# Kernel tuning notes

Hardware: AMD Instinct MI355X
Metric: run time of the kernel (lower is better)

Reference implementation:

```python
import jax, jax.numpy as jnp
import numpy as np

B, T, D, H = 2, 2048, 1024, 16
HD = D // H  # 64
SCALE = 1.0 / np.sqrt(D).astype(np.float32)  # module uses 1/sqrt(mod_dim), not head_dim


def setup_inputs() -> dict:
    key = jax.random.key(0)
    k1, k2, k3 = jax.random.split(key, 3)
    x = jax.random.normal(k1, (B, T, D), dtype=jnp.float32)
    W_attn = jax.random.normal(k2, (3 * D, D), dtype=jnp.float32) * 0.02
    W_out = jax.random.normal(k3, (D, D), dtype=jnp.float32) * 0.02
    return {"x": x, "W_attn": W_attn, "W_out": W_out}


def reference(x, W_attn, W_out):
    b, t, d = x.shape
    # qkv projection (Linear, no bias): x @ W^T
    qkv = jnp.einsum('btd,ed->bte', x, W_attn)  # [b, t, 3d]
    q, k, v = jnp.split(qkv, 3, axis=-1)
    # [b, h, t, hd]
    q = q.reshape(b, t, H, HD).transpose(0, 2, 1, 3)
    k = k.reshape(b, t, H, HD).transpose(0, 2, 1, 3)
    v = v.reshape(b, t, H, HD).transpose(0, 2, 1, 3)
    # raw scores, causal mask applied before scaling (scale*-inf == -inf, so
    # equivalent to the original mask-then-scale order)
    att = jnp.einsum('bhqd,bhkd->bhqk', q, k)
    causal = jnp.tril(jnp.ones((t, t), dtype=bool))
    att = jnp.where(causal[None, None], att * SCALE, -jnp.inf)
    att = jax.nn.softmax(att, axis=-1)
    z = jnp.einsum('bhqk,bhkd->bhqd', att, v)
    z = z.transpose(0, 2, 1, 3).reshape(b, t, d)
    return jnp.einsum('btd,od->bto', z, W_out)
```

## Files before the change

### kernel.cpp

```cpp
#include <hip/hip_runtime.h>
#include <cstddef>

typedef unsigned short u16;
typedef __attribute__((ext_vector_type(4))) float floatx4;
typedef __attribute__((ext_vector_type(8))) short short8;

#define TT 2048
#define DD 1024
#define NH 16
#define ATT_SCALE (1.0f / 32.0f)
#define PSTR 72

__device__ __forceinline__ u16 f2bf(float f) {
  unsigned u = __builtin_bit_cast(unsigned, f);
  u += 0x7fffu + ((u >> 16) & 1u);
  return (u16)(u >> 16);
}

__device__ __forceinline__ unsigned pack2(float a, float b) {
#if __has_builtin(__builtin_amdgcn_cvt_pk_bf16_f32)
  auto t = __builtin_amdgcn_cvt_pk_bf16_f32(a, b);
  return __builtin_bit_cast(unsigned, t);
#else
  unsigned ua = __builtin_bit_cast(unsigned, a);
  ua += 0x7fffu + ((ua >> 16) & 1u);
  unsigned ub = __builtin_bit_cast(unsigned, b);
  ub += 0x7fffu + ((ub >> 16) & 1u);
  return (ua >> 16) | (ub & 0xffff0000u);
#endif
}

__device__ __forceinline__ void g2l16(const u16* g, u16* l) {
#if __has_builtin(__builtin_amdgcn_global_load_lds)
  __builtin_amdgcn_global_load_lds(
      (const __attribute__((address_space(1))) unsigned int*)g,
      (__attribute__((address_space(3))) unsigned int*)l, 16, 0, 0);
#else
  *(int4*)l = *(const int4*)g;
#endif
}

__device__ __forceinline__ short8 scale_q(short8 q) {
  short8 r;
#pragma unroll
  for (int i = 0; i < 8; ++i) {
    float f = __builtin_bit_cast(float, ((unsigned)(u16)q[i]) << 16) * ATT_SCALE;
    r[i] = (short)f2bf(f);
  }
  return r;
}

__global__ __launch_bounds__(256) void cvt3_kernel(const float* __restrict__ a,
                                                   const float* __restrict__ b,
                                                   const float* __restrict__ c,
                                                   u16* __restrict__ out,
                                                   int na, int nb, int nc) {
  int i = blockIdx.x * 256 + threadIdx.x;
  const float* src;
  int j;
  if (i < na) { src = a; j = i; }
  else if (i < na + nb) { src = b; j = i - na; }
  else if (i < na + nb + nc) { src = c; j = i - na - nb; }
  else return;
  float4 v = ((const float4*)src)[j];
  ((ushort4*)out)[i] = make_ushort4(f2bf(v.x), f2bf(v.y), f2bf(v.z), f2bf(v.w));
}

template <int MODE, int BN>
__global__ __launch_bounds__(256) void gemm_bt(const u16* __restrict__ A,
                                               const u16* __restrict__ Bm,
                                               void* __restrict__ C,
                                               u16* __restrict__ vt,
                                               int M, int N, int K) {
  constexpr int NT = BN / 32;
  __shared__ u16 As[128 * 32];
  __shared__ u16 Bs[BN * 32];
  const int tid = threadIdx.x;
  const int lane = tid & 63;
  const int wave = tid >> 6;
  const int quad = lane >> 4;
  const int l16 = lane & 15;
  const int wm = (wave >> 1) * 64;
  const int wn = (wave & 1) * (BN / 2);
  const int m0 = blockIdx.x * 128;
  const int n0 = blockIdx.y * BN;

  const int srow = wave * 16 + (lane >> 2);
  const int scol = (lane & 3) * 8;
  const int sl = wave * 512 + lane * 8;

  floatx4 acc[4][NT] = {};

  for (int k0 = 0; k0 < K; k0 += 32) {
    __syncthreads();
    g2l16(&A[(size_t)(m0 + srow) * K + k0 + scol], &As[sl]);
    g2l16(&A[(size_t)(m0 + 64 + srow) * K + k0 + scol], &As[2048 + sl]);
    g2l16(&Bm[(size_t)(n0 + srow) * K + k0 + scol], &Bs[sl]);
    if (BN == 128)
      g2l16(&Bm[(size_t)(n0 + 64 + srow) * K + k0 + scol], &Bs[2048 + sl]);
    __syncthreads();

    short8 af[4];
#pragma unroll
    for (int mt = 0; mt < 4; ++mt)
      af[mt] = *(const short8*)&As[(wm + mt * 16 + l16) * 32 + quad * 8];
#pragma unroll
    for (int nt = 0; nt < NT; ++nt) {
      short8 bf = *(const short8*)&Bs[(wn + nt * 16 + l16) * 32 + quad * 8];
#pragma unroll
      for (int mt = 0; mt < 4; ++mt)
        acc[mt][nt] = __builtin_amdgcn_mfma_f32_16x16x32_bf16(af[mt], bf, acc[mt][nt], 0, 0, 0);
    }
  }

  if (MODE == 2 && n0 >= 2048) {
    const int bidx = m0 >> 11;
    const int tbase = (m0 & 2047) + wm;
#pragma unroll
    for (int mt = 0; mt < 4; ++mt)
#pragma unroll
      for (int nt = 0; nt < NT; ++nt) {
        int gn = n0 + wn + nt * 16 + l16;
        size_t vrow = (size_t)(bidx * 1024 + gn - 2048);
        int t = tbase + mt * 16 + quad * 4;
        uint2 val;
        val.x = pack2(acc[mt][nt][0], acc[mt][nt][1]);
        val.y = pack2(acc[mt][nt][2], acc[mt][nt][3]);
        *(uint2*)&vt[vrow * TT + t] = val;
      }
  } else {
    const int cw = (MODE == 2) ? 2048 : N;
#pragma unroll
    for (int mt = 0; mt < 4; ++mt)
#pragma unroll
      for (int nt = 0; nt < NT; ++nt)
#pragma unroll
        for (int r = 0; r < 4; ++r) {
          int gm = m0 + wm + mt * 16 + quad * 4 + r;
          int gn = n0 + wn + nt * 16 + l16;
          float v = acc[mt][nt][r];
          if (MODE >= 1)
            ((u16*)C)[(size_t)gm * cw + gn] = f2bf(v);
          else
            ((float*)C)[(size_t)gm * cw + gn] = v;
        }
  }
}

__global__ __launch_bounds__(512) void attn_flash5(const u16* __restrict__ qk,
                                                   const u16* __restrict__ vt,
                                                   u16* __restrict__ z) {
  __shared__ u16 Ks[2][64 * PSTR];
  __shared__ u16 Vs[2][64 * PSTR];
  __shared__ u16 Ps[8][16 * PSTR];

  const int tid = threadIdx.x;
  const int lane = tid & 63;
  const int wave = tid >> 6;
  const int qs = wave & 3;
  const int par = wave >> 2;
  const int quad = lane >> 4;
  const int l16 = lane & 15;

  const int p = blockIdx.x;
  const int qtA = p, qtB = 31 - p;
  const int bh = blockIdx.y;
  const int b = bh >> 4, h = bh & 15;

  const size_t bbase = (size_t)b * TT * 2048;
  const u16* qg = qk + bbase + h * 64;
  const u16* kg = qk + bbase + 1024 + h * 64;
  const u16* vtg = vt + (size_t)bh * 64 * TT;

  short8 qfA[2], qfB[2];
  {
    const size_t ra = (size_t)(qtA * 64 + qs * 16 + l16) * 2048;
    const size_t rb = (size_t)(qtB * 64 + qs * 16 + l16) * 2048;
    qfA[0] = scale_q(*(const short8*)&qg[ra + quad * 8]);
    qfA[1] = scale_q(*(const short8*)&qg[ra + 32 + quad * 8]);
    qfB[0] = scale_q(*(const short8*)&qg[rb + quad * 8]);
    qfB[1] = scale_q(*(const short8*)&qg[rb + 32 + quad * 8]);
  }

  floatx4 OA[4] = {}, OB[4] = {};
  float psA[4] = {}, psB[4] = {};

  const int tsel = tid >> 8;
  const int t8 = tid & 255;
  const int str = t8 >> 2, sc = (t8 & 3) * 16;

  const int nktB = qtB + 1;
  const int M = (nktB + 1) >> 1;
  const int qrbA = qtA * 64 + qs * 16 + quad * 4;
  const int qrbB = qtB * 64 + qs * 16 + quad * 4;

  for (int m = 0; m < M; ++m) {
    const int kt = 2 * m + par;
    const int kt0 = kt * 64;
    __syncthreads();
    {
      const int kst = 2 * m + tsel;
      if (kst < nktB) {
        *(int4*)&Ks[tsel][str * PSTR + sc] =
            *(const int4*)&kg[(size_t)(kst * 64 + str) * 2048 + sc];
        *(int4*)&Ks[tsel][str * PSTR + sc + 8] =
            *(const int4*)&kg[(size_t)(kst * 64 + str) * 2048 + sc + 8];
        *(int4*)&Vs[tsel][str * PSTR + sc] =
            *(const int4*)&vtg[(size_t)str * TT + kst * 64 + sc];
        *(int4*)&Vs[tsel][str * PSTR + sc + 8] =
            *(const int4*)&vtg[(size_t)str * TT + kst * 64 + sc + 8];
      }
    }
    __syncthreads();

    if (kt < nktB) {
      floatx4 s[4];
#pragma unroll
      for (int nt = 0; nt < 4; ++nt) {
        short8 k0 = *(const short8*)&Ks[par][(nt * 16 + l16) * PSTR + quad * 8];
        short8 k1 = *(const short8*)&Ks[par][(nt * 16 + l16) * PSTR + 32 + quad * 8];
        floatx4 zz = {0.f, 0.f, 0.f, 0.f};
        s[nt] = __builtin_amdgcn_mfma_f32_16x16x32_bf16(qfB[0], k0, zz, 0, 0, 0);
        s[nt] = __builtin_amdgcn_mfma_f32_16x16x32_bf16(qfB[1], k1, s[nt], 0, 0, 0);
      }
      if (kt == qtB) {
#pragma unroll
        for (int nt = 0; nt < 4; ++nt)
#pragma unroll
          for (int r = 0; r < 4; ++r) {
            int kk = kt0 + nt * 16 + l16;
            float pv = (kk <= qrbB + r) ? __expf(s[nt][r]) : 0.f;
            psB[r] += pv;
            Ps[wave][(quad * 4 + r) * PSTR + nt * 16 + l16] = f2bf(pv);
          }
      } else {
#pragma unroll
        for (int nt = 0; nt < 4; ++nt)
#pragma unroll
          for (int r = 0; r < 4; ++r) {
            float pv = __expf(s[nt][r]);
            psB[r] += pv;
            Ps[wave][(quad * 4 + r) * PSTR + nt * 16 + l16] = f2bf(pv);
          }
      }
      {
        short8 p0 = *(const short8*)&Ps[wave][l16 * PSTR + quad * 8];
        short8 p1 = *(const short8*)&Ps[wave][l16 * PSTR + 32 + quad * 8];
#pragma unroll
        for (int nt = 0; nt < 4; ++nt) {
          short8 v0 = *(const short8*)&Vs[par][(nt * 16 + l16) * PSTR + quad * 8];
          short8 v1 = *(const short8*)&Vs[par][(nt * 16 + l16) * PSTR + 32 + quad * 8];
          OB[nt] = __builtin_amdgcn_mfma_f32_16x16x32_bf16(p0, v0, OB[nt], 0, 0, 0);
          OB[nt] = __builtin_amdgcn_mfma_f32_16x16x32_bf16(p1, v1, OB[nt], 0, 0, 0);
        }
      }

      if (kt <= qtA) {
#pragma unroll
        for (int nt = 0; nt < 4; ++nt) {
          short8 k0 = *(const short8*)&Ks[par][(nt * 16 + l16) * PSTR + quad * 8];
          short8 k1 = *(const short8*)&Ks[par][(nt * 16 + l16) * PSTR + 32 + quad * 8];
          floatx4 zz = {0.f, 0.f, 0.f, 0.f};
          s[nt] = __builtin_amdgcn_mfma_f32_16x16x32_bf16(qfA[0], k0, zz, 0, 0, 0);
          s[nt] = __builtin_amdgcn_mfma_f32_16x16x32_bf16(qfA[1], k1, s[nt], 0, 0, 0);
        }
        if (kt == qtA) {
#pragma unroll
          for (int nt = 0; nt < 4; ++nt)
#pragma unroll
            for (int r = 0; r < 4; ++r) {
              int kk = kt0 + nt * 16 + l16;
              float pv = (kk <= qrbA + r) ? __expf(s[nt][r]) : 0.f;
              psA[r] += pv;
              Ps[wave][(quad * 4 + r) * PSTR + nt * 16 + l16] = f2bf(pv);
            }
        } else {
#pragma unroll
          for (int nt = 0; nt < 4; ++nt)
#pragma unroll
            for (int r = 0; r < 4; ++r) {
              float pv = __expf(s[nt][r]);
              psA[r] += pv;
              Ps[wave][(quad * 4 + r) * PSTR + nt * 16 + l16] = f2bf(pv);
            }
        }
        short8 p0 = *(const short8*)&Ps[wave][l16 * PSTR + quad * 8];
        short8 p1 = *(const short8*)&Ps[wave][l16 * PSTR + 32 + quad * 8];
#pragma unroll
        for (int nt = 0; nt < 4; ++nt) {
          short8 v0 = *(const short8*)&Vs[par][(nt * 16 + l16) * PSTR + quad * 8];
          short8 v1 = *(const short8*)&Vs[par][(nt * 16 + l16) * PSTR + 32 + quad * 8];
          OA[nt] = __builtin_amdgcn_mfma_f32_16x16x32_bf16(p0, v0, OA[nt], 0, 0, 0);
          OA[nt] = __builtin_amdgcn_mfma_f32_16x16x32_bf16(p1, v1, OA[nt], 0, 0, 0);
        }
      }
    }
  }

#pragma unroll
  for (int off = 1; off < 16; off <<= 1)
#pragma unroll
    for (int r = 0; r < 4; ++r) {
      psA[r] += __shfl_xor(psA[r], off, 64);
      psB[r] += __shfl_xor(psB[r], off, 64);
    }

  float* red = (float*)Ps;
  float* lred = red + 4096;
  __syncthreads();
  if (par == 1) {
#pragma unroll
    for (int nt = 0; nt < 4; ++nt)
#pragma unroll
      for (int r = 0; r < 4; ++r)
        red[(qs * 16 + quad * 4 + r) * 64 + nt * 16 + l16] = OA[nt][r];
    if (l16 == 0)
#pragma unroll
      for (int r = 0; r < 4; ++r) lred[qs * 16 + quad * 4 + r] = psA[r];
  }
  __syncthreads();
  if (par == 0) {
#pragma unroll
    for (int r = 0; r < 4; ++r) {
      int row = qs * 16 + quad * 4 + r;
      float rl = 1.0f / (psA[r] + lred[row]);
      int qa = qtA * 64 + row;
#pragma unroll
      for (int nt = 0; nt < 4; ++nt) {
        float o = OA[nt][r] + red[row * 64 + nt * 16 + l16];
        z[(size_t)(b * TT + qa) * DD + h * 64 + nt * 16 + l16] = f2bf(o * rl);
      }
    }
  }
  __syncthreads();
  if (par == 1) {
#pragma unroll
    for (int nt = 0; nt < 4; ++nt)
#pragma unroll
      for (int r = 0; r < 4; ++r)
        red[(qs * 16 + quad * 4 + r) * 64 + nt * 16 + l16] = OB[nt][r];
    if (l16 == 0)
#pragma unroll
      for (int r = 0; r < 4; ++r) lred[qs * 16 + quad * 4 + r] = psB[r];
  }
  __syncthreads();
  if (par == 0) {
#pragma unroll
    for (int r = 0; r < 4; ++r) {
      int row = qs * 16 + quad * 4 + r;
      float rl = 1.0f / (psB[r] + lred[row]);
      int qb = qtB * 64 + row;
#pragma unroll
      for (int nt = 0; nt < 4; ++nt) {
        float o = OB[nt][r] + red[row * 64 + nt * 16 + l16];
        z[(size_t)(b * TT + qb) * DD + h * 64 + nt * 16 + l16] = f2bf(o * rl);
      }
    }
  }
}

extern "C" void kernel_launch(void* const* d_in, const int* in_sizes, int n_in,
                              void* d_out, int out_size, void* d_ws, size_t ws_size,
                              hipStream_t stream) {
  const float* x  = (const float*)d_in[0];
  const float* Wa = (const float*)d_in[1];
  const float* Wo = (const float*)d_in[2];
  float* out = (float*)d_out;

  u16* xb  = (u16*)d_ws;
  u16* Wab = xb  + (size_t)4096 * 1024;
  u16* Wob = Wab + (size_t)3072 * 1024;
  u16* qk  = Wob + (size_t)1024 * 1024;
  u16* z   = qk  + (size_t)4096 * 2048;
  u16* vt  = z   + (size_t)4096 * 1024;

  cvt3_kernel<<<8192, 256, 0, stream>>>(x, Wa, Wo, xb, 1048576, 786432, 262144);

  gemm_bt<2, 128><<<dim3(32, 24), 256, 0, stream>>>(xb, Wab, qk, vt, 4096, 3072, 1024);

  attn_flash5<<<dim3(16, 2 * NH), 512, 0, stream>>>(qk, vt, z);

  gemm_bt<0, 64><<<dim3(32, 16), 256, 0, stream>>>(z, Wob, out, nullptr, 4096, 1024, 1024);
}
```

Measured before the change: 179.3 us.

## Keep P in registers via bpermute, swizzle K/V LDS, compute S transposed

The attention kernel now computes S transposed (K as the A operand), so each lane holds four consecutive key columns. It packs exp values to bf16 in registers and redistributes them into the PV A-fragment with ds_bpermute, which removes the per-wave P round trip through shared memory. K/V tiles use an XOR-swizzled unpadded layout instead of padding, and setprio hints are placed around MFMA blocks. Row sums become a scalar per lane with a shorter shuffle reduction, and the epilogue reuses the K/V buffers. This trades LDS stores and loads for extra bpermute and select instructions.

```diff
diff --git a/kernel.cpp b/kernel.cpp
--- a/kernel.cpp
+++ b/kernel.cpp
@@ -4,12 +4,12 @@
 typedef unsigned short u16;
 typedef __attribute__((ext_vector_type(4))) float floatx4;
 typedef __attribute__((ext_vector_type(8))) short short8;
+typedef __attribute__((ext_vector_type(4))) unsigned int uintx4;
 
 #define TT 2048
 #define DD 1024
 #define NH 16
 #define ATT_SCALE (1.0f / 32.0f)
-#define PSTR 72
 
 __device__ __forceinline__ u16 f2bf(float f) {
   unsigned u = __builtin_bit_cast(unsigned, f);
@@ -147,12 +147,54 @@
   }
 }
 
-__global__ __launch_bounds__(512) void attn_flash5(const u16* __restrict__ qk,
-                                                   const u16* __restrict__ vt,
-                                                   u16* __restrict__ z) {
-  __shared__ u16 Ks[2][64 * PSTR];
-  __shared__ u16 Vs[2][64 * PSTR];
-  __shared__ u16 Ps[8][16 * PSTR];
+template <bool DIAG>
+__device__ __forceinline__ void exp_pack(const floatx4* s, int kt0, int quad,
+                                         int qr, float& ps, unsigned W[4][2]) {
+#pragma unroll
+  for (int nt = 0; nt < 4; ++nt) {
+    float e[4];
+#pragma unroll
+    for (int r = 0; r < 4; ++r) {
+      float v = __expf(s[nt][r]);
+      if (DIAG) {
+        int kk = kt0 + nt * 16 + quad * 4 + r;
+        v = (kk <= qr) ? v : 0.f;
+      }
+      ps += v;
+      e[r] = v;
+    }
+    W[nt][0] = pack2(e[0], e[1]);
+    W[nt][1] = pack2(e[2], e[3]);
+  }
+}
+
+__device__ __forceinline__ void pfrag(const unsigned W[4][2], int bpA, int bpB,
+                                      int quad, short8& pa0, short8& pa1) {
+  uintx4 a, b;
+#pragma unroll
+  for (int c = 0; c < 2; ++c) {
+    unsigned x0 = (unsigned)__builtin_amdgcn_ds_bpermute(bpA, (int)W[0][c]);
+    unsigned x1 = (unsigned)__builtin_amdgcn_ds_bpermute(bpA, (int)W[1][c]);
+    unsigned y0 = (unsigned)__builtin_amdgcn_ds_bpermute(bpB, (int)W[0][c]);
+    unsigned y1 = (unsigned)__builtin_amdgcn_ds_bpermute(bpB, (int)W[1][c]);
+    a[c]     = (quad < 2) ? x0 : x1;
+    a[2 + c] = (quad < 2) ? y0 : y1;
+    unsigned u0 = (unsigned)__builtin_amdgcn_ds_bpermute(bpA, (int)W[2][c]);
+    unsigned u1 = (unsigned)__builtin_amdgcn_ds_bpermute(bpA, (int)W[3][c]);
+    unsigned t0 = (unsigned)__builtin_amdgcn_ds_bpermute(bpB, (int)W[2][c]);
+    unsigned t1 = (unsigned)__builtin_amdgcn_ds_bpermute(bpB, (int)W[3][c]);
+    b[c]     = (quad < 2) ? u0 : u1;
+    b[2 + c] = (quad < 2) ? t0 : t1;
+  }
+  pa0 = __builtin_bit_cast(short8, a);
+  pa1 = __builtin_bit_cast(short8, b);
+}
+
+__global__ __launch_bounds__(512, 4) void attn_flash6(const u16* __restrict__ qk,
+                                                      const u16* __restrict__ vt,
+                                                      u16* __restrict__ z) {
+  __shared__ u16 Ks[2][64 * 64];
+  __shared__ u16 Vs[2][64 * 64];
 
   const int tid = threadIdx.x;
   const int lane = tid & 63;
@@ -183,16 +225,23 @@
   }
 
   floatx4 OA[4] = {}, OB[4] = {};
-  float psA[4] = {}, psB[4] = {};
+  float psA = 0.f, psB = 0.f;
 
   const int tsel = tid >> 8;
   const int t8 = tid & 255;
   const int str = t8 >> 2, sc = (t8 & 3) * 16;
+  const int swr = (str & 7) << 3;
 
   const int nktB = qtB + 1;
   const int M = (nktB + 1) >> 1;
-  const int qrbA = qtA * 64 + qs * 16 + quad * 4;
-  const int qrbB = qtB * 64 + qs * 16 + quad * 4;
+  const int qrA = qtA * 64 + qs * 16 + l16;
+  const int qrB = qtB * 64 + qs * 16 + l16;
+
+  const int sw = (l16 & 7) << 3;
+  const int rc0 = (quad * 8) ^ sw;
+  const int rc1 = (32 + quad * 8) ^ sw;
+  const int bpA = ((((lane >> 4) & 1) << 5) | l16) << 2;
+  const int bpB = bpA + 64;
 
   for (int m = 0; m < M; ++m) {
     const int kt = 2 * m + par;
@@ -201,13 +250,13 @@
     {
       const int kst = 2 * m + tsel;
       if (kst < nktB) {
-        *(int4*)&Ks[tsel][str * PSTR + sc] =
+        *(int4*)&Ks[tsel][str * 64 + (sc ^ swr)] =
             *(const int4*)&kg[(size_t)(kst * 64 + str) * 2048 + sc];
-        *(int4*)&Ks[tsel][str * PSTR + sc + 8] =
+        *(int4*)&Ks[tsel][str * 64 + ((sc + 8) ^ swr)] =
             *(const int4*)&kg[(size_t)(kst * 64 + str) * 2048 + sc + 8];
-        *(int4*)&Vs[tsel][str * PSTR + sc] =
+        *(int4*)&Vs[tsel][str * 64 + (sc ^ swr)] =
             *(const int4*)&vtg[(size_t)str * TT + kst * 64 + sc];
-        *(int4*)&Vs[tsel][str * PSTR + sc + 8] =
+        *(int4*)&Vs[tsel][str * 64 + ((sc + 8) ^ swr)] =
             *(const int4*)&vtg[(size_t)str * TT + kst * 64 + sc + 8];
       }
     }
@@ -215,98 +264,79 @@
 
     if (kt < nktB) {
       floatx4 s[4];
+      __builtin_amdgcn_s_setprio(1);
 #pragma unroll
       for (int nt = 0; nt < 4; ++nt) {
-        short8 k0 = *(const short8*)&Ks[par][(nt * 16 + l16) * PSTR + quad * 8];
-        short8 k1 = *(const short8*)&Ks[par][(nt * 16 + l16) * PSTR + 32 + quad * 8];
+        const int ro = (nt * 16 + l16) * 64;
+        short8 k0 = *(const short8*)&Ks[par][ro + rc0];
+        short8 k1 = *(const short8*)&Ks[par][ro + rc1];
         floatx4 zz = {0.f, 0.f, 0.f, 0.f};
-        s[nt] = __builtin_amdgcn_mfma_f32_16x16x32_bf16(qfB[0], k0, zz, 0, 0, 0);
-        s[nt] = __builtin_amdgcn_mfma_f32_16x16x32_bf16(qfB[1], k1, s[nt], 0, 0, 0);
-      }
-      if (kt == qtB) {
-#pragma unroll
-        for (int nt = 0; nt < 4; ++nt)
-#pragma unroll
-          for (int r = 0; r < 4; ++r) {
-            int kk = kt0 + nt * 16 + l16;
-            float pv = (kk <= qrbB + r) ? __expf(s[nt][r]) : 0.f;
-            psB[r] += pv;
-            Ps[wave][(quad * 4 + r) * PSTR + nt * 16 + l16] = f2bf(pv);
-          }
-      } else {
-#pragma unroll
-        for (int nt = 0; nt < 4; ++nt)
-#pragma unroll
-          for (int r = 0; r < 4; ++r) {
-            float pv = __expf(s[nt][r]);
-            psB[r] += pv;
-            Ps[wave][(quad * 4 + r) * PSTR + nt * 16 + l16] = f2bf(pv);
-          }
-      }
+        s[nt] = __builtin_amdgcn_mfma_f32_16x16x32_bf16(k0, qfB[0], zz, 0, 0, 0);
+        s[nt] = __builtin_amdgcn_mfma_f32_16x16x32_bf16(k1, qfB[1], s[nt], 0, 0, 0);
+      }
+      __builtin_amdgcn_s_setprio(0);
+      short8 pa0, pa1;
       {
-        short8 p0 = *(const short8*)&Ps[wave][l16 * PSTR + quad * 8];
-        short8 p1 = *(const short8*)&Ps[wave][l16 * PSTR + 32 + quad * 8];
+        unsigned W[4][2];
+        if (kt == qtB)
+          exp_pack<true>(s, kt0, quad, qrB, psB, W);
+        else
+          exp_pack<false>(s, kt0, quad, qrB, psB, W);
+        pfrag(W, bpA, bpB, quad, pa0, pa1);
+      }
+      __builtin_amdgcn_s_setprio(1);
+#pragma unroll
+      for (int nt = 0; nt < 4; ++nt) {
+        const int ro = (nt * 16 + l16) * 64;
+        short8 v0 = *(const short8*)&Vs[par][ro + rc0];
+        short8 v1 = *(const short8*)&Vs[par][ro + rc1];
+        OB[nt] = __builtin_amdgcn_mfma_f32_16x16x32_bf16(pa0, v0, OB[nt], 0, 0, 0);
+        OB[nt] = __builtin_amdgcn_mfma_f32_16x16x32_bf16(pa1, v1, OB[nt], 0, 0, 0);
+      }
+      __builtin_amdgcn_s_setprio(0);
+
+      if (kt <= qtA) {
+        __builtin_amdgcn_s_setprio(1);
 #pragma unroll
         for (int nt = 0; nt < 4; ++nt) {
-          short8 v0 = *(const short8*)&Vs[par][(nt * 16 + l16) * PSTR + quad * 8];
-          short8 v1 = *(const short8*)&Vs[par][(nt * 16 + l16) * PSTR + 32 + quad * 8];
-          OB[nt] = __builtin_amdgcn_mfma_f32_16x16x32_bf16(p0, v0, OB[nt], 0, 0, 0);
-          OB[nt] = __builtin_amdgcn_mfma_f32_16x16x32_bf16(p1, v1, OB[nt], 0, 0, 0);
+          const int ro = (nt * 16 + l16) * 64;
+          short8 k0 = *(const short8*)&Ks[par][ro + rc0];
+          short8 k1 = *(const short8*)&Ks[par][ro + rc1];
+          floatx4 zz = {0.f, 0.f, 0.f, 0.f};
+          s[nt] = __builtin_amdgcn_mfma_f32_16x16x32_bf16(k0, qfA[0], zz, 0, 0, 0);
+          s[nt] = __builtin_amdgcn_mfma_f32_16x16x32_bf16(k1, qfA[1], s[nt], 0, 0, 0);
         }
-      }
-
-      if (kt <= qtA) {
+        __builtin_amdgcn_s_setprio(0);
+        {
+          unsigned W[4][2];
+          if (kt == qtA)
+            exp_pack<true>(s, kt0, quad, qrA, psA, W);
+          else
+            exp_pack<false>(s, kt0, quad, qrA, psA, W);
+          pfrag(W, bpA, bpB, quad, pa0, pa1);
+        }
+        __builtin_amdgcn_s_setprio(1);
 #pragma unroll
         for (int nt = 0; nt < 4; ++nt) {
-          short8 k0 = *(const short8*)&Ks[par][(nt * 16 + l16) * PSTR + quad * 8];
-          short8 k1 = *(const short8*)&Ks[par][(nt * 16 + l16) * PSTR + 32 + quad * 8];
-          floatx4 zz = {0.f, 0.f, 0.f, 0.f};
-          s[nt] = __builtin_amdgcn_mfma_f32_16x16x32_bf16(qfA[0], k0, zz, 0, 0, 0);
-          s[nt] = __builtin_amdgcn_mfma_f32_16x16x32_bf16(qfA[1], k1, s[nt], 0, 0, 0);
+          const int ro = (nt * 16 + l16) * 64;
+          short8 v0 = *(const short8*)&Vs[par][ro + rc0];
+          short8 v1 = *(const short8*)&Vs[par][ro + rc1];
+          OA[nt] = __builtin_amdgcn_mfma_f32_16x16x32_bf16(pa0, v0, OA[nt], 0, 0, 0);
+          OA[nt] = __builtin_amdgcn_mfma_f32_16x16x32_bf16(pa1, v1, OA[nt], 0, 0, 0);
         }
-        if (kt == qtA) {
-#pragma unroll
-          for (int nt = 0; nt < 4; ++nt)
-#pragma unroll
-            for (int r = 0; r < 4; ++r) {
-              int kk = kt0 + nt * 16 + l16;
-              float pv = (kk <= qrbA + r) ? __expf(s[nt][r]) : 0.f;
-              psA[r] += pv;
-              Ps[wave][(quad * 4 + r) * PSTR + nt * 16 + l16] = f2bf(pv);
-            }
-        } else {
-#pragma unroll
-          for (int nt = 0; nt < 4; ++nt)
-#pragma unroll
-            for (int r = 0; r < 4; ++r) {
-              float pv = __expf(s[nt][r]);
-              psA[r] += pv;
-              Ps[wave][(quad * 4 + r) * PSTR + nt * 16 + l16] = f2bf(pv);
-            }
-        }
-        short8 p0 = *(const short8*)&Ps[wave][l16 * PSTR + quad * 8];
-        short8 p1 = *(const short8*)&Ps[wave][l16 * PSTR + 32 + quad * 8];
-#pragma unroll
-        for (int nt = 0; nt < 4; ++nt) {
-          short8 v0 = *(const short8*)&Vs[par][(nt * 16 + l16) * PSTR + quad * 8];
-          short8 v1 = *(const short8*)&Vs[par][(nt * 16 + l16) * PSTR + 32 + quad * 8];
-          OA[nt] = __builtin_amdgcn_mfma_f32_16x16x32_bf16(p0, v0, OA[nt], 0, 0, 0);
-          OA[nt] = __builtin_amdgcn_mfma_f32_16x16x32_bf16(p1, v1, OA[nt], 0, 0, 0);
-        }
-      }
-    }
-  }
-
-#pragma unroll
-  for (int off = 1; off < 16; off <<= 1)
-#pragma unroll
-    for (int r = 0; r < 4; ++r) {
-      psA[r] += __shfl_xor(psA[r], off, 64);
-      psB[r] += __shfl_xor(psB[r], off, 64);
-    }
-
-  float* red = (float*)Ps;
-  float* lred = red + 4096;
+        __builtin_amdgcn_s_setprio(0);
+      }
+    }
+  }
+
+  psA += __shfl_xor(psA, 16);
+  psA += __shfl_xor(psA, 32);
+  psB += __shfl_xor(psB, 16);
+  psB += __shfl_xor(psB, 32);
+
+  float* red = (float*)Ks;
+  float* lred = (float*)Vs;
+
   __syncthreads();
   if (par == 1) {
 #pragma unroll
@@ -314,16 +344,14 @@
 #pragma unroll
       for (int r = 0; r < 4; ++r)
         red[(qs * 16 + quad * 4 + r) * 64 + nt * 16 + l16] = OA[nt][r];
-    if (l16 == 0)
-#pragma unroll
-      for (int r = 0; r < 4; ++r) lred[qs * 16 + quad * 4 + r] = psA[r];
-  }
+  }
+  if (quad == 0) lred[par * 64 + qs * 16 + l16] = psA;
   __syncthreads();
   if (par == 0) {
 #pragma unroll
     for (int r = 0; r < 4; ++r) {
       int row = qs * 16 + quad * 4 + r;
-      float rl = 1.0f / (psA[r] + lred[row]);
+      float rl = 1.0f / (lred[row] + lred[64 + row]);
       int qa = qtA * 64 + row;
 #pragma unroll
       for (int nt = 0; nt < 4; ++nt) {
@@ -339,16 +367,14 @@
 #pragma unroll
       for (int r = 0; r < 4; ++r)
         red[(qs * 16 + quad * 4 + r) * 64 + nt * 16 + l16] = OB[nt][r];
-    if (l16 == 0)
-#pragma unroll
-      for (int r = 0; r < 4; ++r) lred[qs * 16 + quad * 4 + r] = psB[r];
-  }
+  }
+  if (quad == 0) lred[par * 64 + qs * 16 + l16] = psB;
   __syncthreads();
   if (par == 0) {
 #pragma unroll
     for (int r = 0; r < 4; ++r) {
       int row = qs * 16 + quad * 4 + r;
-      float rl = 1.0f / (psB[r] + lred[row]);
+      float rl = 1.0f / (lred[row] + lred[64 + row]);
       int qb = qtB * 64 + row;
 #pragma unroll
       for (int nt = 0; nt < 4; ++nt) {
@@ -378,7 +404,7 @@
 
   gemm_bt<2, 128><<<dim3(32, 24), 256, 0, stream>>>(xb, Wab, qk, vt, 4096, 3072, 1024);
 
-  attn_flash5<<<dim3(16, 2 * NH), 512, 0, stream>>>(qk, vt, z);
+  attn_flash6<<<dim3(16, 2 * NH), 512, 0, stream>>>(qk, vt, z);
 
   gemm_bt<0, 64><<<dim3(32, 16), 256, 0, stream>>>(z, Wob, out, nullptr, 4096, 1024, 1024);
 }
```

Result: no change. 180.0 us (+0.4%).
